# Optimization experiments

Measured on AMD Instinct MI355X. Metric: run time of the kernel, lower is better.

## Reference

```python
import jax, jax.numpy as jnp
import numpy as np

H = 256          # LSTM hidden size
P = 1            # proj_size
L = 5            # num LSTM layers
T = 1000         # sequence length (forced by Linear(1000, 100))


def _uniform(key, shape, scale):
    return jax.random.uniform(key, shape, dtype=jnp.float32, minval=-scale, maxval=scale)


def setup_inputs() -> dict:
    key = jax.random.key(0)
    ks = jax.random.split(key, 16)
    B = 128
    s = 1.0 / np.sqrt(H)  # PyTorch LSTM init scale
    inp = {
        "x": jax.random.normal(ks[0], (B, T, 1), dtype=jnp.float32),
        # stacked LSTM params: layer input dim is 1 for all layers (input_size=1, proj_size=1)
        "Wih": _uniform(ks[1], (L, 4 * H, 1), s),
        "Whh": _uniform(ks[2], (L, 4 * H, P), s),
        "bih": _uniform(ks[3], (L, 4 * H), s),
        "bhh": _uniform(ks[4], (L, 4 * H), s),
        "Whr": _uniform(ks[5], (L, P, H), s),
        # MLP head
        "W1": _uniform(ks[6], (100, 1000), 1.0 / np.sqrt(1000)),
        "b1": _uniform(ks[7], (100,), 1.0 / np.sqrt(1000)),
        "W2": _uniform(ks[8], (100, 100), 0.1),
        "b2": _uniform(ks[9], (100,), 0.1),
        "W3": _uniform(ks[10], (100, 100), 0.1),
        "b3": _uniform(ks[11], (100,), 0.1),
        "W4": _uniform(ks[12], (1, 100), 0.1),
        "b4": _uniform(ks[13], (1,), 0.1),
    }
    return inp


def _lstm_layer(x_seq, Wih, Whh, bih, bhh, Whr):
    """One projected LSTM layer. x_seq: [B, T, in_dim] -> [B, T, P]."""
    B = x_seq.shape[0]
    # precompute input contribution for all timesteps: [B, T, 4H]
    gx = jnp.einsum('bti,gi->btg', x_seq, Wih) + bih + bhh
    gx = jnp.transpose(gx, (1, 0, 2))  # [T, B, 4H] for scan

    def step(carry, g_t):
        h, c = carry                      # h: [B, P], c: [B, H]
        gates = g_t + h @ Whh.T           # [B, 4H]
        i = jax.nn.sigmoid(gates[:, 0 * H:1 * H])
        f = jax.nn.sigmoid(gates[:, 1 * H:2 * H])
        g = jnp.tanh(gates[:, 2 * H:3 * H])
        o = jax.nn.sigmoid(gates[:, 3 * H:4 * H])
        c = f * c + i * g
        h = (o * jnp.tanh(c)) @ Whr.T     # projected hidden: [B, P]
        return (h, c), h

    h0 = jnp.zeros((B, P), x_seq.dtype)
    c0 = jnp.zeros((B, H), x_seq.dtype)
    _, hs = jax.lax.scan(step, (h0, c0), gx)  # hs: [T, B, P]
    return jnp.transpose(hs, (1, 0, 2))       # [B, T, P]


def reference(x, Wih, Whh, bih, bhh, Whr, W1, b1, W2, b2, W3, b3, W4, b4):
    out = x
    for l in range(L):  # fixed 5 stacked layers
        out = _lstm_layer(out, Wih[l], Whh[l], bih[l], bhh[l], Whr[l])
    out = out[:, :, 0]                      # squeeze -> [B, 1000]
    out = jax.nn.sigmoid(out @ W1.T + b1)   # linear1 + Sigmoid
    out = jax.nn.sigmoid(out @ W2.T + b2)   # linear2 + Sigmoid
    out = jax.nn.relu(out @ W3.T + b3)      # linear3 + ReLU
    out = out @ W4.T + b4                   # linear4 -> [B, 1]
    return out
```

## Files before the change

kernel.cpp:

```cpp
#include <hip/hip_runtime.h>


#define LAYERS 5
#define TT 1000
#define BATCH 128
#define CH 40
#define NCH (TT / CH)

#define LOG2E 1.4426950408889634f

__device__ __forceinline__ float fast_exp2(float x) {
#if __has_builtin(__builtin_amdgcn_exp2f)
  return __builtin_amdgcn_exp2f(x);
#else
  return __exp2f(x);
#endif
}
__device__ __forceinline__ float fast_rcp(float x) {
#if __has_builtin(__builtin_amdgcn_rcpf)
  return __builtin_amdgcn_rcpf(x);
#else
  return 1.0f / x;
#endif
}
__device__ __forceinline__ float fast_sigmoid(float z) {
  float e = fast_exp2(-LOG2E * z);
  return fast_rcp(1.0f + e);
}

template <int CTRL>
__device__ __forceinline__ float dpp_add(float v) {
  int moved = __builtin_amdgcn_update_dpp(0, __builtin_bit_cast(int, v),
                                          CTRL, 0xF, 0xF, false);
  return v + __builtin_bit_cast(float, moved);
}

__device__ __forceinline__ float wave_sum_uniform(float v) {
  v = dpp_add<0x128>(v);
  v = dpp_add<0x124>(v);
  v = dpp_add<0x122>(v);
  v = dpp_add<0x121>(v);
  v = dpp_add<0x142>(v);
  v = dpp_add<0x143>(v);
  return __builtin_bit_cast(float, __builtin_amdgcn_readlane(__builtin_bit_cast(int, v), 63));
}

__device__ __forceinline__ float lane_bcast(float v, int s) {
  return __builtin_bit_cast(float, __builtin_amdgcn_readlane(__builtin_bit_cast(int, v), s));
}

__global__ __launch_bounds__(64, 1) void lstm_wave_kernel(
    const float* __restrict__ x,
    const float* __restrict__ Wih,
    const float* __restrict__ Whh,
    const float* __restrict__ bih,
    const float* __restrict__ bhh,
    const float* __restrict__ Whr,
    const float* __restrict__ W1, const float* __restrict__ b1,
    const float* __restrict__ W2, const float* __restrict__ b2,
    const float* __restrict__ W3, const float* __restrict__ b3,
    const float* __restrict__ W4, const float* __restrict__ b4,
    float* __restrict__ out,
    float* __restrict__ seq,
    int* __restrict__ flags)
{
  __shared__ float sx[TT];
  __shared__ float sh[104];
  __shared__ float sh2[104];

  const int bid  = blockIdx.x;
  const int l    = bid >> 7;
  const int b    = bid & 127;
  const int lane = threadIdx.x;

  float wix[4][4], whx[4][4], gb[4][4], whr[4], cc[4];
  const int base = l * 1024;
#pragma unroll
  for (int g = 0; g < 4; ++g) {
    const float sc = (g == 2) ? (-2.0f * LOG2E) : (-LOG2E);
#pragma unroll
    for (int k = 0; k < 4; ++k) {
      int j = base + g * 256 + k * 64 + lane;
      wix[g][k] = Wih[j] * sc;
      whx[g][k] = Whh[j] * sc;
      gb[g][k]  = (bih[j] + bhh[j]) * sc;
    }
  }
#pragma unroll
  for (int k = 0; k < 4; ++k) {
    whr[k] = Whr[l * 256 + k * 64 + lane];
    cc[k] = 0.0f;
  }

  const float* in  = (l == 0) ? (x + b * TT) : (seq + ((l - 1) * BATCH + b) * TT);
  float*       outp = seq + (l * BATCH + b) * TT;
  int*       my_flag = flags + l * BATCH + b;
  const int* in_flag = (l > 0) ? (flags + (l - 1) * BATCH + b) : (const int*)flags;

  const float M4 = -4.0f * LOG2E;
  const float P2 =  2.0f * LOG2E;

  float h = 0.0f;
  for (int c = 0; c < NCH; ++c) {
    if (l > 0) {
      while (__hip_atomic_load(in_flag, __ATOMIC_ACQUIRE,
                               __HIP_MEMORY_SCOPE_AGENT) <= c)
        __builtin_amdgcn_s_sleep(2);
    }
    float xv = 0.0f;
    if (lane < CH) {
      if (l == 0)
        xv = in[c * CH + lane];
      else
        xv = __hip_atomic_load(in + c * CH + lane, __ATOMIC_RELAXED,
                               __HIP_MEMORY_SCOPE_AGENT);
    }

    float outv = 0.0f;
#pragma unroll 2
    for (int s = 0; s < CH; ++s) {
      const float xs = lane_bcast(xv, s);

      float gx[4][4];
#pragma unroll
      for (int g = 0; g < 4; ++g)
#pragma unroll
        for (int k = 0; k < 4; ++k)
          gx[g][k] = fmaf(xs, wix[g][k], gb[g][k]);

      float E[4][4];
#pragma unroll
      for (int g = 0; g < 4; ++g)
#pragma unroll
        for (int k = 0; k < 4; ++k)
          E[g][k] = fast_exp2(fmaf(h, whx[g][k], gx[g][k]));

      float r0, r1, r2, r3;
      {
        float rr[4];
#pragma unroll
        for (int k = 0; k < 4; ++k) {
          float ig = fast_rcp(1.0f + E[0][k]);
          float fg = fast_rcp(1.0f + E[1][k]);
          float gg = fmaf(2.0f, fast_rcp(1.0f + E[2][k]), -1.0f);
          float og = fast_rcp(1.0f + E[3][k]);
          cc[k] = fmaf(fg, cc[k], ig * gg);
          float tE = fast_exp2(cc[k] * (-2.0f * LOG2E));
          float tc = fmaf(2.0f, fast_rcp(1.0f + tE), -1.0f);
          rr[k] = og * tc * whr[k];
        }
        r0 = rr[0]; r1 = rr[1]; r2 = rr[2]; r3 = rr[3];
      }
      float r = (r0 + r1) + (r2 + r3);

      h = wave_sum_uniform(r);
      if (lane == s) outv = h;
      if (l == 4 && lane == 0) sx[c * CH + s] = h;
    }

    if (l < 4) {
      if (lane < CH)
        __hip_atomic_store(outp + c * CH + lane, outv, __ATOMIC_RELAXED,
                           __HIP_MEMORY_SCOPE_AGENT);
      if (lane == 0)
        __hip_atomic_store(my_flag, c + 1, __ATOMIC_RELEASE,
                           __HIP_MEMORY_SCOPE_AGENT);
    }
    (void)outv;
  }

  if (l != 4) return;

  __syncthreads();

#pragma unroll
  for (int oo = 0; oo < 2; ++oo) {
    const int o = lane + oo * 64;
    if (o < 100) {
      const float* w = W1 + o * TT;
      float s0 = 0.f, s1 = 0.f, s2 = 0.f, s3 = 0.f;
      for (int t = 0; t < TT; t += 4) {
        float4 v = *(const float4*)(w + t);
        s0 = fmaf(v.x, sx[t + 0], s0);
        s1 = fmaf(v.y, sx[t + 1], s1);
        s2 = fmaf(v.z, sx[t + 2], s2);
        s3 = fmaf(v.w, sx[t + 3], s3);
      }
      sh[o] = fast_sigmoid((s0 + s1) + (s2 + s3) + b1[o]);
    }
  }
  __syncthreads();

#pragma unroll
  for (int oo = 0; oo < 2; ++oo) {
    const int o = lane + oo * 64;
    if (o < 100) {
      const float* w = W2 + o * 100;
      float acc = b2[o];
      for (int k = 0; k < 100; k += 4) {
        float4 v = *(const float4*)(w + k);
        acc = fmaf(v.x, sh[k + 0], acc);
        acc = fmaf(v.y, sh[k + 1], acc);
        acc = fmaf(v.z, sh[k + 2], acc);
        acc = fmaf(v.w, sh[k + 3], acc);
      }
      sh2[o] = fast_sigmoid(acc);
    }
  }
  __syncthreads();

#pragma unroll
  for (int oo = 0; oo < 2; ++oo) {
    const int o = lane + oo * 64;
    if (o < 100) {
      const float* w = W3 + o * 100;
      float acc = b3[o];
      for (int k = 0; k < 100; k += 4) {
        float4 v = *(const float4*)(w + k);
        acc = fmaf(v.x, sh2[k + 0], acc);
        acc = fmaf(v.y, sh2[k + 1], acc);
        acc = fmaf(v.z, sh2[k + 2], acc);
        acc = fmaf(v.w, sh2[k + 3], acc);
      }
      sx[o] = fmaxf(acc, 0.0f);
    }
  }
  __syncthreads();

  float r = 0.0f;
#pragma unroll
  for (int oo = 0; oo < 2; ++oo) {
    const int o = lane + oo * 64;
    if (o < 100) r = fmaf(sx[o], W4[o], r);
  }
  r = wave_sum_uniform(r);
  if (lane == 0) out[b] = r + b4[0];
}

extern "C" void kernel_launch(void* const* d_in, const int* in_sizes, int n_in,
                              void* d_out, int out_size, void* d_ws, size_t ws_size,
                              hipStream_t stream) {
  const float* x   = (const float*)d_in[0];
  const float* Wih = (const float*)d_in[1];
  const float* Whh = (const float*)d_in[2];
  const float* bih = (const float*)d_in[3];
  const float* bhh = (const float*)d_in[4];
  const float* Whr = (const float*)d_in[5];
  const float* W1  = (const float*)d_in[6];
  const float* b1  = (const float*)d_in[7];
  const float* W2  = (const float*)d_in[8];
  const float* b2  = (const float*)d_in[9];
  const float* W3  = (const float*)d_in[10];
  const float* b3  = (const float*)d_in[11];
  const float* W4  = (const float*)d_in[12];
  const float* b4  = (const float*)d_in[13];

  float* seq   = (float*)d_ws;
  int*   flags = (int*)(seq + LAYERS * BATCH * TT);

  hipMemsetAsync(flags, 0, LAYERS * BATCH * sizeof(int), stream);
  lstm_wave_kernel<<<LAYERS * BATCH, 64, 0, stream>>>(
      x, Wih, Whh, bih, bhh, Whr, W1, b1, W2, b2, W3, b3, W4, b4,
      (float*)d_out, seq, flags);
}
```

Measured before the change: 602.1 us.

## Move MLP head into separate consumer blocks pipelined with last LSTM layer

Adds 128 extra blocks that poll the layer-4 chunk flags and accumulate the first linear layer chunk by chunk while the recurrence is still running. The last-layer LSTM blocks now just publish their outputs like the other layers instead of buffering the whole sequence in shared memory and running the MLP at the end. This takes the head's serial tail off the critical path of the slowest recurrence blocks. The cost is more blocks spinning on flags, extra global traffic, and the removal of the occupancy hint from launch bounds.

```diff
diff --git a/kernel.cpp b/kernel.cpp
--- a/kernel.cpp
+++ b/kernel.cpp
@@ -49,7 +49,7 @@
   return __builtin_bit_cast(float, __builtin_amdgcn_readlane(__builtin_bit_cast(int, v), s));
 }
 
-__global__ __launch_bounds__(64, 1) void lstm_wave_kernel(
+__global__ __launch_bounds__(64) void lstm_fused_kernel(
     const float* __restrict__ x,
     const float* __restrict__ Wih,
     const float* __restrict__ Whh,
@@ -60,105 +60,98 @@
     const float* __restrict__ W2, const float* __restrict__ b2,
     const float* __restrict__ W3, const float* __restrict__ b3,
     const float* __restrict__ W4, const float* __restrict__ b4,
-    float* __restrict__ out,
+    float* __restrict__ y,
     float* __restrict__ seq,
     int* __restrict__ flags)
 {
-  __shared__ float sx[TT];
-  __shared__ float sh[104];
-  __shared__ float sh2[104];
-
   const int bid  = blockIdx.x;
-  const int l    = bid >> 7;
-  const int b    = bid & 127;
   const int lane = threadIdx.x;
 
-  float wix[4][4], whx[4][4], gb[4][4], whr[4], cc[4];
-  const int base = l * 1024;
-#pragma unroll
-  for (int g = 0; g < 4; ++g) {
-    const float sc = (g == 2) ? (-2.0f * LOG2E) : (-LOG2E);
+  if (bid < LAYERS * BATCH) {
+    const int l = bid >> 7;
+    const int b = bid & 127;
+
+    float wix[4][4], whx[4][4], gb[4][4], whr[4], cc[4];
+    const int base = l * 1024;
+#pragma unroll
+    for (int g = 0; g < 4; ++g) {
+      const float sc = (g == 2) ? (-2.0f * LOG2E) : (-LOG2E);
+#pragma unroll
+      for (int k = 0; k < 4; ++k) {
+        int j = base + g * 256 + k * 64 + lane;
+        wix[g][k] = Wih[j] * sc;
+        whx[g][k] = Whh[j] * sc;
+        gb[g][k]  = (bih[j] + bhh[j]) * sc;
+      }
+    }
 #pragma unroll
     for (int k = 0; k < 4; ++k) {
-      int j = base + g * 256 + k * 64 + lane;
-      wix[g][k] = Wih[j] * sc;
-      whx[g][k] = Whh[j] * sc;
-      gb[g][k]  = (bih[j] + bhh[j]) * sc;
-    }
-  }
-#pragma unroll
-  for (int k = 0; k < 4; ++k) {
-    whr[k] = Whr[l * 256 + k * 64 + lane];
-    cc[k] = 0.0f;
-  }
-
-  const float* in  = (l == 0) ? (x + b * TT) : (seq + ((l - 1) * BATCH + b) * TT);
-  float*       outp = seq + (l * BATCH + b) * TT;
-  int*       my_flag = flags + l * BATCH + b;
-  const int* in_flag = (l > 0) ? (flags + (l - 1) * BATCH + b) : (const int*)flags;
-
-  const float M4 = -4.0f * LOG2E;
-  const float P2 =  2.0f * LOG2E;
-
-  float h = 0.0f;
-  for (int c = 0; c < NCH; ++c) {
-    if (l > 0) {
-      while (__hip_atomic_load(in_flag, __ATOMIC_ACQUIRE,
-                               __HIP_MEMORY_SCOPE_AGENT) <= c)
-        __builtin_amdgcn_s_sleep(2);
-    }
-    float xv = 0.0f;
-    if (lane < CH) {
-      if (l == 0)
-        xv = in[c * CH + lane];
-      else
-        xv = __hip_atomic_load(in + c * CH + lane, __ATOMIC_RELAXED,
-                               __HIP_MEMORY_SCOPE_AGENT);
-    }
-
-    float outv = 0.0f;
+      whr[k] = Whr[l * 256 + k * 64 + lane];
+      cc[k] = 0.0f;
+    }
+
+    const float* in   = (l == 0) ? (x + b * TT) : (seq + ((l - 1) * BATCH + b) * TT);
+    float*       outp = seq + (l * BATCH + b) * TT;
+    int*       my_flag = flags + l * BATCH + b;
+    const int* in_flag = (l > 0) ? (flags + (l - 1) * BATCH + b) : (const int*)flags;
+
+    float h = 0.0f;
+    for (int c = 0; c < NCH; ++c) {
+      if (l > 0) {
+        while (__hip_atomic_load(in_flag, __ATOMIC_ACQUIRE,
+                                 __HIP_MEMORY_SCOPE_AGENT) <= c)
+          __builtin_amdgcn_s_sleep(2);
+      }
+      float xv = 0.0f;
+      if (lane < CH) {
+        if (l == 0)
+          xv = in[c * CH + lane];
+        else
+          xv = __hip_atomic_load(in + c * CH + lane, __ATOMIC_RELAXED,
+                                 __HIP_MEMORY_SCOPE_AGENT);
+      }
+
+      float outv = 0.0f;
 #pragma unroll 2
-    for (int s = 0; s < CH; ++s) {
-      const float xs = lane_bcast(xv, s);
-
-      float gx[4][4];
-#pragma unroll
-      for (int g = 0; g < 4; ++g)
-#pragma unroll
-        for (int k = 0; k < 4; ++k)
-          gx[g][k] = fmaf(xs, wix[g][k], gb[g][k]);
-
-      float E[4][4];
-#pragma unroll
-      for (int g = 0; g < 4; ++g)
-#pragma unroll
-        for (int k = 0; k < 4; ++k)
-          E[g][k] = fast_exp2(fmaf(h, whx[g][k], gx[g][k]));
-
-      float r0, r1, r2, r3;
-      {
-        float rr[4];
-#pragma unroll
-        for (int k = 0; k < 4; ++k) {
-          float ig = fast_rcp(1.0f + E[0][k]);
-          float fg = fast_rcp(1.0f + E[1][k]);
-          float gg = fmaf(2.0f, fast_rcp(1.0f + E[2][k]), -1.0f);
-          float og = fast_rcp(1.0f + E[3][k]);
-          cc[k] = fmaf(fg, cc[k], ig * gg);
-          float tE = fast_exp2(cc[k] * (-2.0f * LOG2E));
-          float tc = fmaf(2.0f, fast_rcp(1.0f + tE), -1.0f);
-          rr[k] = og * tc * whr[k];
+      for (int s = 0; s < CH; ++s) {
+        const float xs = lane_bcast(xv, s);
+
+        float gx[4][4];
+#pragma unroll
+        for (int g = 0; g < 4; ++g)
+#pragma unroll
+          for (int k = 0; k < 4; ++k)
+            gx[g][k] = fmaf(xs, wix[g][k], gb[g][k]);
+
+        float E[4][4];
+#pragma unroll
+        for (int g = 0; g < 4; ++g)
+#pragma unroll
+          for (int k = 0; k < 4; ++k)
+            E[g][k] = fast_exp2(fmaf(h, whx[g][k], gx[g][k]));
+
+        float r0, r1, r2, r3;
+        {
+          float rr[4];
+#pragma unroll
+          for (int k = 0; k < 4; ++k) {
+            float ig = fast_rcp(1.0f + E[0][k]);
+            float fg = fast_rcp(1.0f + E[1][k]);
+            float gg = fmaf(2.0f, fast_rcp(1.0f + E[2][k]), -1.0f);
+            float og = fast_rcp(1.0f + E[3][k]);
+            cc[k] = fmaf(fg, cc[k], ig * gg);
+            float tE = fast_exp2(cc[k] * (-2.0f * LOG2E));
+            float tc = fmaf(2.0f, fast_rcp(1.0f + tE), -1.0f);
+            rr[k] = og * tc * whr[k];
+          }
+          r0 = rr[0]; r1 = rr[1]; r2 = rr[2]; r3 = rr[3];
         }
-        r0 = rr[0]; r1 = rr[1]; r2 = rr[2]; r3 = rr[3];
-      }
-      float r = (r0 + r1) + (r2 + r3);
-
-      h = wave_sum_uniform(r);
-      if (lane == s) outv = h;
-      if (l == 4 && lane == 0) sx[c * CH + s] = h;
-    }
-
-    if (l < 4) {
+        float r = (r0 + r1) + (r2 + r3);
+
+        h = wave_sum_uniform(r);
+        if (lane == s) outv = h;
+      }
+
       if (lane < CH)
         __hip_atomic_store(outp + c * CH + lane, outv, __ATOMIC_RELAXED,
                            __HIP_MEMORY_SCOPE_AGENT);
@@ -166,75 +159,88 @@
         __hip_atomic_store(my_flag, c + 1, __ATOMIC_RELEASE,
                            __HIP_MEMORY_SCOPE_AGENT);
     }
-    (void)outv;
-  }
-
-  if (l != 4) return;
-
+    return;
+  }
+
+  __shared__ float sh[100];
+  __shared__ float sh2[100];
+  __shared__ float sh3[100];
+
+  const int b = bid - LAYERS * BATCH;
+  const int o0 = lane;
+  const int o1 = lane + 50;
+
+  const int*   f4 = flags + 4 * BATCH + b;
+  const float* h4 = seq + (4 * BATCH + b) * TT;
+
+  float acc0 = 0.0f, acc1 = 0.0f;
+  for (int c = 0; c < NCH; ++c) {
+    while (__hip_atomic_load(f4, __ATOMIC_ACQUIRE,
+                             __HIP_MEMORY_SCOPE_AGENT) <= c)
+      __builtin_amdgcn_s_sleep(8);
+    if (lane < 50) {
+      const float* w0 = W1 + o0 * TT + c * CH;
+      const float* w1 = W1 + o1 * TT + c * CH;
+      const float* hh = h4 + c * CH;
+#pragma unroll
+      for (int t = 0; t < CH; t += 4) {
+        float4 hv = *(const float4*)(hh + t);
+        float4 a  = *(const float4*)(w0 + t);
+        float4 bq = *(const float4*)(w1 + t);
+        acc0 = fmaf(a.x, hv.x, acc0);  acc1 = fmaf(bq.x, hv.x, acc1);
+        acc0 = fmaf(a.y, hv.y, acc0);  acc1 = fmaf(bq.y, hv.y, acc1);
+        acc0 = fmaf(a.z, hv.z, acc0);  acc1 = fmaf(bq.z, hv.z, acc1);
+        acc0 = fmaf(a.w, hv.w, acc0);  acc1 = fmaf(bq.w, hv.w, acc1);
+      }
+    }
+  }
+
+  if (lane < 50) {
+    sh[o0] = fast_sigmoid(acc0 + b1[o0]);
+    sh[o1] = fast_sigmoid(acc1 + b1[o1]);
+  }
   __syncthreads();
 
-#pragma unroll
-  for (int oo = 0; oo < 2; ++oo) {
-    const int o = lane + oo * 64;
-    if (o < 100) {
-      const float* w = W1 + o * TT;
-      float s0 = 0.f, s1 = 0.f, s2 = 0.f, s3 = 0.f;
-      for (int t = 0; t < TT; t += 4) {
-        float4 v = *(const float4*)(w + t);
-        s0 = fmaf(v.x, sx[t + 0], s0);
-        s1 = fmaf(v.y, sx[t + 1], s1);
-        s2 = fmaf(v.z, sx[t + 2], s2);
-        s3 = fmaf(v.w, sx[t + 3], s3);
-      }
-      sh[o] = fast_sigmoid((s0 + s1) + (s2 + s3) + b1[o]);
-    }
+  if (lane < 50) {
+    float a0 = b2[o0], a1 = b2[o1];
+    const float* w0 = W2 + o0 * 100;
+    const float* w1 = W2 + o1 * 100;
+#pragma unroll 5
+    for (int k = 0; k < 100; k += 4) {
+      float4 v0 = *(const float4*)(w0 + k);
+      float4 v1 = *(const float4*)(w1 + k);
+      a0 = fmaf(v0.x, sh[k + 0], a0);  a1 = fmaf(v1.x, sh[k + 0], a1);
+      a0 = fmaf(v0.y, sh[k + 1], a0);  a1 = fmaf(v1.y, sh[k + 1], a1);
+      a0 = fmaf(v0.z, sh[k + 2], a0);  a1 = fmaf(v1.z, sh[k + 2], a1);
+      a0 = fmaf(v0.w, sh[k + 3], a0);  a1 = fmaf(v1.w, sh[k + 3], a1);
+    }
+    sh2[o0] = fast_sigmoid(a0);
+    sh2[o1] = fast_sigmoid(a1);
   }
   __syncthreads();
 
-#pragma unroll
-  for (int oo = 0; oo < 2; ++oo) {
-    const int o = lane + oo * 64;
-    if (o < 100) {
-      const float* w = W2 + o * 100;
-      float acc = b2[o];
-      for (int k = 0; k < 100; k += 4) {
-        float4 v = *(const float4*)(w + k);
-        acc = fmaf(v.x, sh[k + 0], acc);
-        acc = fmaf(v.y, sh[k + 1], acc);
-        acc = fmaf(v.z, sh[k + 2], acc);
-        acc = fmaf(v.w, sh[k + 3], acc);
-      }
-      sh2[o] = fast_sigmoid(acc);
-    }
+  if (lane < 50) {
+    float a0 = b3[o0], a1 = b3[o1];
+    const float* w0 = W3 + o0 * 100;
+    const float* w1 = W3 + o1 * 100;
+#pragma unroll 5
+    for (int k = 0; k < 100; k += 4) {
+      float4 v0 = *(const float4*)(w0 + k);
+      float4 v1 = *(const float4*)(w1 + k);
+      a0 = fmaf(v0.x, sh2[k + 0], a0);  a1 = fmaf(v1.x, sh2[k + 0], a1);
+      a0 = fmaf(v0.y, sh2[k + 1], a0);  a1 = fmaf(v1.y, sh2[k + 1], a1);
+      a0 = fmaf(v0.z, sh2[k + 2], a0);  a1 = fmaf(v1.z, sh2[k + 2], a1);
+      a0 = fmaf(v0.w, sh2[k + 3], a0);  a1 = fmaf(v1.w, sh2[k + 3], a1);
+    }
+    sh3[o0] = fmaxf(a0, 0.0f);
+    sh3[o1] = fmaxf(a1, 0.0f);
   }
   __syncthreads();
 
-#pragma unroll
-  for (int oo = 0; oo < 2; ++oo) {
-    const int o = lane + oo * 64;
-    if (o < 100) {
-      const float* w = W3 + o * 100;
-      float acc = b3[o];
-      for (int k = 0; k < 100; k += 4) {
-        float4 v = *(const float4*)(w + k);
-        acc = fmaf(v.x, sh2[k + 0], acc);
-        acc = fmaf(v.y, sh2[k + 1], acc);
-        acc = fmaf(v.z, sh2[k + 2], acc);
-        acc = fmaf(v.w, sh2[k + 3], acc);
-      }
-      sx[o] = fmaxf(acc, 0.0f);
-    }
-  }
-  __syncthreads();
-
   float r = 0.0f;
-#pragma unroll
-  for (int oo = 0; oo < 2; ++oo) {
-    const int o = lane + oo * 64;
-    if (o < 100) r = fmaf(sx[o], W4[o], r);
-  }
+  if (lane < 50) r = fmaf(sh3[o0], W4[o0], sh3[o1] * W4[o1]);
   r = wave_sum_uniform(r);
-  if (lane == 0) out[b] = r + b4[0];
+  if (lane == 0) y[b] = r + b4[0];
 }
 
 extern "C" void kernel_launch(void* const* d_in, const int* in_sizes, int n_in,
@@ -259,7 +265,7 @@
   int*   flags = (int*)(seq + LAYERS * BATCH * TT);
 
   hipMemsetAsync(flags, 0, LAYERS * BATCH * sizeof(int), stream);
-  lstm_wave_kernel<<<LAYERS * BATCH, 64, 0, stream>>>(
+  lstm_fused_kernel<<<LAYERS * BATCH + BATCH, 64, 0, stream>>>(
       x, Wih, Whh, bih, bhh, Whr, W1, b1, W2, b2, W3, b3, W4, b4,
       (float*)d_out, seq, flags);
 }
```

New measurement: 734.7 us. 22.0% more time.
